# Kernel optimization log

Measured on AMD Instinct MI355X. Metric: run time of the kernel, lower is better.

The kernel has to match this reference:

```python
import jax, jax.numpy as jnp
import numpy as np

TAU = 0.03        # self.tau
EPS = 0.65       # args.epsilon
EPS2 = 0.4       # args.epsilon2 (trimap)
LOGIT_T = 0.07    # logits temperature


def _l2norm(x, axis):
    # torch F.normalize: x / max(||x||, 1e-12)
    n = jnp.sqrt(jnp.sum(x * x, axis=axis, keepdims=True))
    return x / jnp.maximum(n, 1e-12)


def setup_inputs() -> dict:
    key = jax.random.key(0)
    k1, k2 = jax.random.split(key)
    img = jax.random.normal(k1, (256, 512, 14, 14), dtype=jnp.float32)
    aud = jax.random.normal(k2, (256, 512), dtype=jnp.float32)
    return {"img": img, "aud": aud}


def reference(img, aud):
    # img: [B, C, H, W] backbone vision features; aud: [B, C] pooled audio features
    B = img.shape[0]
    img = _l2norm(img, axis=1)
    aud = _l2norm(aud, axis=1)

    # A: paired audio-visual correlation map [B, 1, H, W]
    A = jnp.einsum('nchw,nc->nhw', img, aud)[:, None]
    # A0: full cross-pair correlation maps [B, B, H, W] (n = image idx, m = audio idx)
    A0 = jnp.einsum('nchw,mc->nmhw', img, aud)
    # AdaptiveMaxPool2d((1,1)) -> max over spatial dims -> [B, B]
    A0_ref = jnp.max(A0, axis=(2, 3))

    Pos = jax.nn.sigmoid((A - EPS) / TAU)           # [B, 1, H, W]
    Pos2 = jax.nn.sigmoid((A - EPS2) / TAU)         # trimap branch
    Neg = 1.0 - Pos2
    Pos_all = jax.nn.sigmoid((A0 - EPS) / TAU)      # [B, B, H, W]

    mask = 1.0 - 100.0 * jnp.eye(B, dtype=img.dtype)
    # gated weighted-mean pooling over spatial dims
    sim = (Pos_all * A0).sum(axis=(2, 3)) / Pos_all.sum(axis=(2, 3)) * mask   # [B, B]
    sim1 = (Pos * A).sum(axis=(2, 3)) / Pos.sum(axis=(2, 3))                  # [B, 1]
    sim2 = (Neg * A).sum(axis=(2, 3)) / Neg.sum(axis=(2, 3))                  # [B, 1]

    logits = jnp.concatenate((sim1, sim, sim2), axis=1) / LOGIT_T             # [B, B+2]
    return (A, logits, Pos, Neg, A0_ref)
```

## Files before the change

kernel.cpp:

```cpp
#include <hip/hip_runtime.h>
#include <math.h>

typedef _Float16 half8 __attribute__((ext_vector_type(8)));
typedef float f32x4 __attribute__((ext_vector_type(4)));

#define HWN 196
#define RLT (1.0f/0.07f)


__global__ __launch_bounds__(256) void prep_aud_pk(const float* __restrict__ aud,
                                                   _Float16* __restrict__ aud_pk) {
    int m = blockIdx.x, t = threadIdx.x;
    float a0 = aud[m * 512 + t];
    float a1 = aud[m * 512 + 256 + t];
    float s = a0 * a0 + a1 * a1;
    #pragma unroll
    for (int off = 32; off; off >>= 1) s += __shfl_down(s, off, 64);
    __shared__ float wsum[4];
    __shared__ float rns;
    if ((t & 63) == 0) wsum[t >> 6] = s;
    __syncthreads();
    if (t == 0) rns = 1.0f / fmaxf(sqrtf(wsum[0] + wsum[1] + wsum[2] + wsum[3]), 1e-12f);
    __syncthreads();
    float rn = rns;
    int c0 = t, c1 = t + 256;
    aud_pk[(c0 >> 3) * 2048 + m * 8 + (c0 & 7)] = (_Float16)(a0 * rn);
    aud_pk[(c1 >> 3) * 2048 + m * 8 + (c1 & 7)] = (_Float16)(a1 * rn);
}

__global__ __launch_bounds__(512, 2) void av_mfma(const float* __restrict__ img,
                                                  const _Float16* __restrict__ aud_pk,
                                                  float* __restrict__ out) {
    const int n = blockIdx.x;
    const int tid = threadIdx.x;
    const int w = tid >> 6, l = tid & 63;
    const int q = w & 3;
    const int hh = w >> 2;
    const int HT = hh ? 6 : 7;

    __shared__ _Float16 __align__(16) Abuf[2][4][208][8];
    __shared__ _Float16 __align__(16) Bbuf[2][4][256][8];
    __shared__ float rnorm_s[208];
    __shared__ float nrm_parts[2][196];
    __shared__ float red_max[2][256], red_sw[2][256], red_swa[2][256];
    __shared__ float diag_parts[2][4][4];

    if (tid < 96) {
        int b = tid / 48, rem = tid % 48, kg = rem / 12, row = 196 + rem % 12;
        *(float4*)&Abuf[b][kg][row][0] = make_float4(0.f, 0.f, 0.f, 0.f);
    }

    const float* imgn = img + (size_t)n * (512 * 196);
    const bool act = tid < 392;
    const int cl  = act ? tid / 196 : 0;
    const int hws = act ? tid % 196 : 0;
    float nrm = 0.f;

    float  av[16];
    float4 bv[2];

    {
        if (act) {
            #pragma unroll
            for (int i = 0; i < 16; i++) av[i] = imgn[(cl + 2 * i) * 196 + hws];
        }
        const float4* bs = (const float4*)aud_pk + tid;
        bv[0] = bs[0]; bv[1] = bs[512];
        if (act) {
            #pragma unroll
            for (int i = 0; i < 16; i++) {
                int c = cl + 2 * i;
                nrm += av[i] * av[i];
                Abuf[0][c >> 3][hws][c & 7] = (_Float16)av[i];
            }
        }
        ((float4*)&Bbuf[0][0][0][0])[tid]       = bv[0];
        ((float4*)&Bbuf[0][0][0][0])[tid + 512] = bv[1];
    }
    __syncthreads();

    f32x4 acc[7][4];
    #pragma unroll
    for (int ht = 0; ht < 7; ht++)
        #pragma unroll
        for (int mt = 0; mt < 4; mt++)
            acc[ht][mt] = (f32x4){0.f, 0.f, 0.f, 0.f};

    const int aoff = (l >> 4) * 1664 + (hh * 112 + (l & 15)) * 8;
    const int boff = (l >> 4) * 2048 + (q * 64 + (l & 15)) * 8;

    for (int t = 0; t < 16; t++) {
        const int cur = t & 1;
        const bool more = t < 15;
        if (more) {
            const float* src = imgn + (t + 1) * 32 * 196;
            if (act) {
                #pragma unroll
                for (int i = 0; i < 16; i++) av[i] = src[(cl + 2 * i) * 196 + hws];
            }
            const float4* bs = (const float4*)aud_pk + (t + 1) * 1024 + tid;
            bv[0] = bs[0]; bv[1] = bs[512];
        }
        {
            const _Float16* Ab = &Abuf[cur][0][0][0];
            const _Float16* Bb = &Bbuf[cur][0][0][0];
            half8 bfrag[4];
            #pragma unroll
            for (int mt = 0; mt < 4; mt++) bfrag[mt] = *(const half8*)(Bb + boff + mt * 128);
            half8 afrag[7];
            #pragma unroll
            for (int ht = 0; ht < 7; ht++)
                if (ht < HT) afrag[ht] = *(const half8*)(Ab + aoff + ht * 128);
            #pragma unroll
            for (int ht = 0; ht < 7; ht++)
                if (ht < HT)
                    #pragma unroll
                    for (int mt = 0; mt < 4; mt++)
                        acc[ht][mt] = __builtin_amdgcn_mfma_f32_16x16x32_f16(
                            afrag[ht], bfrag[mt], acc[ht][mt], 0, 0, 0);
        }
        if (more) {
            const int nb = cur ^ 1;
            if (act) {
                #pragma unroll
                for (int i = 0; i < 16; i++) {
                    int c = cl + 2 * i;
                    nrm += av[i] * av[i];
                    Abuf[nb][c >> 3][hws][c & 7] = (_Float16)av[i];
                }
            }
            ((float4*)&Bbuf[nb][0][0][0])[tid]       = bv[0];
            ((float4*)&Bbuf[nb][0][0][0])[tid + 512] = bv[1];
        }
        __syncthreads();
    }

    if (act) nrm_parts[cl][hws] = nrm;
    __syncthreads();
    if (tid < 208) {
        float v = 0.f;
        if (tid < 196) {
            float s = nrm_parts[0][tid] + nrm_parts[1][tid];
            v = 1.0f / fmaxf(sqrtf(s), 1e-12f);
        }
        rnorm_s[tid] = v;
    }
    __syncthreads();

    float mx[4], sw[4], swa[4];
    #pragma unroll
    for (int mt = 0; mt < 4; mt++) { mx[mt] = -1e30f; sw[mt] = 0.f; swa[mt] = 0.f; }
    float s1n = 0.f, s1d = 0.f, s2n = 0.f, s2d = 0.f;
    const int dmt = (n >> 4) & 3, dq = n >> 6, dl = n & 15;
    const bool isdiag = (q == dq) && ((l & 15) == dl);

    #pragma unroll
    for (int ht = 0; ht < 7; ht++) {
        if (ht < HT) {
            int rowb = hh * 112 + ht * 16 + ((l >> 4) << 2);
            #pragma unroll
            for (int r = 0; r < 4; r++) {
                int hw = rowb + r;
                float rn = rnorm_s[hw];
                bool valid = hw < 196;
                #pragma unroll
                for (int mt = 0; mt < 4; mt++) {
                    float a0 = acc[ht][mt][r] * rn;
                    if (valid) {
                        float wg = 1.0f / (1.0f + __expf((0.65f - a0) * (1.0f / 0.03f)));
                        mx[mt]  = fmaxf(mx[mt], a0);
                        sw[mt] += wg;
                        swa[mt] += wg * a0;
                        if (isdiag && mt == dmt) {
                            out[n * 196 + hw] = a0;
                            out[116224 + n * 196 + hw] = wg;
                            float p2 = 1.0f / (1.0f + __expf((0.40f - a0) * (1.0f / 0.03f)));
                            float ng = 1.0f - p2;
                            out[166400 + n * 196 + hw] = ng;
                            s1n += wg * a0; s1d += wg;
                            s2n += ng * a0; s2d += ng;
                        }
                    }
                }
            }
        }
    }

    #pragma unroll
    for (int mt = 0; mt < 4; mt++) {
        float m1 = mx[mt], v1 = sw[mt], v2 = swa[mt];
        m1 = fmaxf(m1, __shfl_xor(m1, 16, 64)); v1 += __shfl_xor(v1, 16, 64); v2 += __shfl_xor(v2, 16, 64);
        m1 = fmaxf(m1, __shfl_xor(m1, 32, 64)); v1 += __shfl_xor(v1, 32, 64); v2 += __shfl_xor(v2, 32, 64);
        if (l < 16) {
            int m = q * 64 + mt * 16 + l;
            red_max[hh][m] = m1; red_sw[hh][m] = v1; red_swa[hh][m] = v2;
        }
    }
    if (isdiag) {
        diag_parts[hh][l >> 4][0] = s1n;
        diag_parts[hh][l >> 4][1] = s1d;
        diag_parts[hh][l >> 4][2] = s2n;
        diag_parts[hh][l >> 4][3] = s2d;
    }
    __syncthreads();

    if (tid < 256) {
        int m = tid;
        float mxv = fmaxf(red_max[0][m], red_max[1][m]);
        float num = red_swa[0][m] + red_swa[1][m];
        float den = red_sw[0][m] + red_sw[1][m];
        float sim = num / den;
        if (m == n) sim *= -99.0f;
        out[50176 + n * 258 + 1 + m] = sim * RLT;
        out[216576 + n * 256 + m] = mxv;
        if (m == n) {
            float t1n = 0.f, t1d = 0.f, t2n = 0.f, t2d = 0.f;
            #pragma unroll
            for (int h2 = 0; h2 < 2; h2++)
                #pragma unroll
                for (int g = 0; g < 4; g++) {
                    t1n += diag_parts[h2][g][0]; t1d += diag_parts[h2][g][1];
                    t2n += diag_parts[h2][g][2]; t2d += diag_parts[h2][g][3];
                }
            out[50176 + n * 258]       = (t1n / t1d) * RLT;
            out[50176 + n * 258 + 257] = (t2n / t2d) * RLT;
        }
    }
}

extern "C" void kernel_launch(void* const* d_in, const int* in_sizes, int n_in,
                              void* d_out, int out_size, void* d_ws, size_t ws_size,
                              hipStream_t stream) {
    const float* img = (const float*)d_in[0];
    const float* aud = (const float*)d_in[1];
    float* out = (float*)d_out;
    _Float16* aud_pk = (_Float16*)d_ws;

    prep_aud_pk<<<256, 256, 0, stream>>>(aud, aud_pk);
    av_mfma<<<256, 512, 0, stream>>>(img, aud_pk, out);
}
```

Before: 47.69 us.

## Stage audio tiles via direct global-to-LDS loads and vectorize image LDS stores

Audio fragment tiles are now copied straight from global memory into shared memory with global_load_lds, so they no longer pass through registers. Each thread now loads 16 consecutive channels instead of strided ones, which lets it pack them into two 16-byte half8 stores rather than 16 scalar half stores. The occupancy hint (min 2 blocks per CU) is dropped from launch_bounds. The goal is to cut register pressure and LDS store instruction count, at the risk of more LDS bank conflicts on the wide stores and changed occupancy.

```diff
diff --git a/kernel.cpp b/kernel.cpp
--- a/kernel.cpp
+++ b/kernel.cpp
@@ -4,9 +4,14 @@
 typedef _Float16 half8 __attribute__((ext_vector_type(8)));
 typedef float f32x4 __attribute__((ext_vector_type(4)));
 
-#define HWN 196
 #define RLT (1.0f/0.07f)
 
+
+__device__ __forceinline__ void gll16(const void* g, void* l) {
+    __builtin_amdgcn_global_load_lds(
+        (const __attribute__((address_space(1))) void*)g,
+        (__attribute__((address_space(3))) void*)l, 16, 0, 0);
+}
 
 __global__ __launch_bounds__(256) void prep_aud_pk(const float* __restrict__ aud,
                                                    _Float16* __restrict__ aud_pk) {
@@ -28,9 +33,9 @@
     aud_pk[(c1 >> 3) * 2048 + m * 8 + (c1 & 7)] = (_Float16)(a1 * rn);
 }
 
-__global__ __launch_bounds__(512, 2) void av_mfma(const float* __restrict__ img,
-                                                  const _Float16* __restrict__ aud_pk,
-                                                  float* __restrict__ out) {
+__global__ __launch_bounds__(512) void av_mfma2(const float* __restrict__ img,
+                                                const _Float16* __restrict__ aud_pk,
+                                                float* __restrict__ out) {
     const int n = blockIdx.x;
     const int tid = threadIdx.x;
     const int w = tid >> 6, l = tid & 63;
@@ -52,31 +57,41 @@
 
     const float* imgn = img + (size_t)n * (512 * 196);
     const bool act = tid < 392;
-    const int cl  = act ? tid / 196 : 0;
+    const int p   = act ? tid / 196 : 0;
     const int hws = act ? tid % 196 : 0;
     float nrm = 0.f;
-
-    float  av[16];
-    float4 bv[2];
-
-    {
-        if (act) {
-            #pragma unroll
-            for (int i = 0; i < 16; i++) av[i] = imgn[(cl + 2 * i) * 196 + hws];
-        }
-        const float4* bs = (const float4*)aud_pk + tid;
-        bv[0] = bs[0]; bv[1] = bs[512];
-        if (act) {
-            #pragma unroll
-            for (int i = 0; i < 16; i++) {
-                int c = cl + 2 * i;
-                nrm += av[i] * av[i];
-                Abuf[0][c >> 3][hws][c & 7] = (_Float16)av[i];
-            }
-        }
-        ((float4*)&Bbuf[0][0][0][0])[tid]       = bv[0];
-        ((float4*)&Bbuf[0][0][0][0])[tid + 512] = bv[1];
-    }
+    float av[16];
+
+    #define STAGE_B(t, buf)                                                        \
+        do {                                                                       \
+            const _Float16* g0 = aud_pk + (((size_t)(t) * 1024 + w * 64 + l) << 3);\
+            _Float16* l0 = &Bbuf[buf][0][0][0] + ((w * 64) << 3);                  \
+            gll16(g0, l0);                                                         \
+            gll16(g0 + 4096, l0 + 4096);                                           \
+        } while (0)
+
+    #define STAGE_A(buf)                                                           \
+        do {                                                                       \
+            if (act) {                                                             \
+                half8 h0, h1;                                                      \
+                _Pragma("unroll")                                                  \
+                for (int i = 0; i < 8; i++) {                                      \
+                    h0[i] = (_Float16)av[i];                                       \
+                    h1[i] = (_Float16)av[8 + i];                                   \
+                    nrm += av[i] * av[i] + av[8 + i] * av[8 + i];                   \
+                }                                                                  \
+                *(half8*)&Abuf[buf][2 * p][hws][0]     = h0;                       \
+                *(half8*)&Abuf[buf][2 * p + 1][hws][0] = h1;                       \
+            }                                                                      \
+        } while (0)
+
+    STAGE_B(0, 0);
+    if (act) {
+        const float* src = imgn + (size_t)(p * 16) * 196 + hws;
+        #pragma unroll
+        for (int i = 0; i < 16; i++) av[i] = src[i * 196];
+    }
+    STAGE_A(0);
     __syncthreads();
 
     f32x4 acc[7][4];
@@ -90,16 +105,15 @@
     const int boff = (l >> 4) * 2048 + (q * 64 + (l & 15)) * 8;
 
     for (int t = 0; t < 16; t++) {
-        const int cur = t & 1;
+        const int cur = t & 1, nb = cur ^ 1;
         const bool more = t < 15;
         if (more) {
-            const float* src = imgn + (t + 1) * 32 * 196;
+            STAGE_B(t + 1, nb);
             if (act) {
+                const float* src = imgn + (size_t)(32 * (t + 1) + p * 16) * 196 + hws;
                 #pragma unroll
-                for (int i = 0; i < 16; i++) av[i] = src[(cl + 2 * i) * 196 + hws];
+                for (int i = 0; i < 16; i++) av[i] = src[i * 196];
             }
-            const float4* bs = (const float4*)aud_pk + (t + 1) * 1024 + tid;
-            bv[0] = bs[0]; bv[1] = bs[512];
         }
         {
             const _Float16* Ab = &Abuf[cur][0][0][0];
@@ -119,23 +133,11 @@
                         acc[ht][mt] = __builtin_amdgcn_mfma_f32_16x16x32_f16(
                             afrag[ht], bfrag[mt], acc[ht][mt], 0, 0, 0);
         }
-        if (more) {
-            const int nb = cur ^ 1;
-            if (act) {
-                #pragma unroll
-                for (int i = 0; i < 16; i++) {
-                    int c = cl + 2 * i;
-                    nrm += av[i] * av[i];
-                    Abuf[nb][c >> 3][hws][c & 7] = (_Float16)av[i];
-                }
-            }
-            ((float4*)&Bbuf[nb][0][0][0])[tid]       = bv[0];
-            ((float4*)&Bbuf[nb][0][0][0])[tid + 512] = bv[1];
-        }
+        if (more) STAGE_A(nb);
         __syncthreads();
     }
 
-    if (act) nrm_parts[cl][hws] = nrm;
+    if (act) nrm_parts[p][hws] = nrm;
     __syncthreads();
     if (tid < 208) {
         float v = 0.f;
@@ -237,5 +239,5 @@
     _Float16* aud_pk = (_Float16*)d_ws;
 
     prep_aud_pk<<<256, 256, 0, stream>>>(aud, aud_pk);
-    av_mfma<<<256, 512, 0, stream>>>(img, aud_pk, out);
-}
+    av_mfma2<<<256, 512, 0, stream>>>(img, aud_pk, out);
+}
```

Measured after the change: 48.58 us. About the same (+1.9%).
